# Optimization experiments

Measured on AMD Instinct MI355X. Metric: run time of the kernel, lower is better.

The kernel has to match this reference:

```python
import jax, jax.numpy as jnp
import numpy as np

DECAY = 0.99
EPS = 1e-05
LOSS_FACTOR = 0.1


def setup_inputs() -> dict:
    key = jax.random.key(0)
    k1, k2, k3, k4 = jax.random.split(key, 4)
    x = jax.random.normal(k1, (64, 256, 32, 32), dtype=jnp.float32)
    centroids = jax.random.normal(k2, (256, 1024), dtype=jnp.float32)
    cluster_size = jax.random.uniform(k3, (1024,), dtype=jnp.float32)
    centroids_avg = jax.random.normal(k4, (256, 1024), dtype=jnp.float32)
    return {"x": x, "centroids": centroids, "cluster_size": cluster_size,
            "centroids_avg": centroids_avg}


def _forward(x, centroids, cluster_size, centroids_avg):
    F, K = centroids.shape
    # torch: x_flat = x.transpose(-1, 1).contiguous().view(-1, n_features)
    xs = jnp.swapaxes(x, 1, -1)              # [B, W, H, C]
    flat_shape = xs.shape
    xf = xs.reshape(-1, F)                   # [N, F]
    dist = ((xf * xf).sum(1, keepdims=True)
            + (centroids * centroids).sum(0, keepdims=True)
            - 2.0 * (xf @ centroids))        # [N, K]
    ind = jnp.argmin(dist, axis=1)           # [N] nearest centroid
    # training-path EMA updates (one-hot matmuls expressed as segment sums)
    counts = jax.ops.segment_sum(jnp.ones(ind.shape, dtype=xf.dtype), ind,
                                 num_segments=K)              # [K]
    centroids_sum = jax.ops.segment_sum(xf, ind, num_segments=K).T  # [F, K]
    new_cs = DECAY * cluster_size + (1.0 - DECAY) * counts
    new_avg = DECAY * centroids_avg + (1.0 - DECAY) * centroids_sum
    n = new_cs.sum()
    cs_norm = (new_cs + EPS) / (n + K * EPS) * n
    new_centroids = new_avg / cs_norm[None, :]               # [F, K]
    # quantize with updated codebook (embedding lookup)
    xq = new_centroids.T[ind].reshape(flat_shape)            # [B, W, H, C]
    xq = jnp.swapaxes(xq, 1, -1)                             # [B, C, H, W]
    xq_st = x + jax.lax.stop_gradient(xq - x)                # straight-through
    return xq_st, xq


def reference(x, centroids, cluster_size, centroids_avg):
    out, _ = _forward(x, centroids, cluster_size, centroids_avg)
    return out
```

## Files before the change

kernel.cpp:

```cpp
#include <hip/hip_runtime.h>


#define DECAY 0.99f
#define EPSF 1e-5f
#define DELTA 0.05f

typedef _Float16 f16x8 __attribute__((ext_vector_type(8)));
typedef float f32x4 __attribute__((ext_vector_type(4)));

static __device__ __forceinline__ unsigned short h_bits(_Float16 h) {
  return __builtin_bit_cast(unsigned short, h);
}
static __device__ __forceinline__ float h_val(unsigned short u) {
  return (float)__builtin_bit_cast(_Float16, u);
}

__global__ void csq_kernel(const float* __restrict__ cent, float* __restrict__ csq) {
  int k0 = blockIdx.x * 64;
  int t = threadIdx.x;
  int kk = t & 63, cg = t >> 6;
  float s = 0.f;
  for (int c = cg; c < 256; c += 4) {
    float v = cent[(size_t)c * 1024 + k0 + kk];
    s += v * v;
  }
  __shared__ float red[4][64];
  red[cg][kk] = s;
  __syncthreads();
  if (t < 64) csq[k0 + t] = red[0][t] + red[1][t] + red[2][t] + red[3][t];
}

__global__ void centT_kernel(const float* __restrict__ cent, _Float16* __restrict__ ctp) {
  __shared__ float tl[32][33];
  int f0 = (blockIdx.x >> 5) * 32, k0 = (blockIdx.x & 31) * 32;
  int t = threadIdx.x;
#pragma unroll
  for (int i = 0; i < 4; ++i) {
    int fi = (t >> 5) + i * 8, ki = t & 31;
    tl[fi][ki] = cent[(size_t)(f0 + fi) * 1024 + k0 + ki];
  }
  __syncthreads();
#pragma unroll
  for (int i = 0; i < 4; ++i) {
    int ki = (t >> 5) + i * 8, fi = t & 31;
    int k = k0 + ki, f = f0 + fi;
    _Float16 h = (_Float16)tl[fi][ki];
    size_t idx = (size_t)(k >> 4) * 4096 + (size_t)(f >> 5) * 512 +
                 (size_t)(k & 15) * 32 + (size_t)((f >> 3) & 3) * 8 + (f & 7);
    ctp[idx] = h;
  }
}

__global__ void transpose_kernel(const float* __restrict__ x, _Float16* __restrict__ xh,
                                 _Float16* __restrict__ xl) {
  __shared__ float tile[64][65];
  int bid = blockIdx.x;
  int pt = bid & 15, ct = (bid >> 4) & 3, b = bid >> 6;
  int c0 = ct * 64, p0 = pt * 64;
  int t = threadIdx.x;
#pragma unroll
  for (int i = 0; i < 16; ++i) {
    int idx = t + i * 256;
    int ci = idx >> 6, pi = idx & 63;
    tile[ci][pi] = x[((size_t)(b * 256 + c0 + ci) << 10) + p0 + pi];
  }
  __syncthreads();
#pragma unroll
  for (int i = 0; i < 8; ++i) {
    int idx = t + i * 256;
    int pi = idx >> 5, cp = idx & 31;
    int p = p0 + pi;
    int r = ((p & 31) << 5) | (p >> 5);
    float v0 = tile[cp * 2][pi], v1 = tile[cp * 2 + 1][pi];
    _Float16 h0 = (_Float16)v0, h1 = (_Float16)v1;
    _Float16 l0 = (_Float16)(v0 - (float)h0), l1 = (_Float16)(v1 - (float)h1);
    unsigned int uh = (unsigned int)h_bits(h0) | ((unsigned int)h_bits(h1) << 16);
    unsigned int ul = (unsigned int)h_bits(l0) | ((unsigned int)h_bits(l1) << 16);
    size_t base = ((size_t)((b << 10) + r)) * 128 + ct * 32 + cp;
    ((unsigned int*)xh)[base] = uh;
    ((unsigned int*)xl)[base] = ul;
  }
}

__global__ __launch_bounds__(256, 2) void mfma_argmin_kernel(
    const _Float16* __restrict__ xh, const _Float16* __restrict__ ctp,
    const float* __restrict__ csq, int* __restrict__ ind,
    int* __restrict__ flaglist, unsigned int* __restrict__ flagcnt,
    unsigned int* __restrict__ counts) {
  __shared__ _Float16 Ah[64 * 256];
  __shared__ _Float16 Bst[4 * 2 * 4 * 512];
  __shared__ float csql[1024];
  __shared__ float red1[4][64], red2[4][64];
  __shared__ int redk[4][64];
  const int t = threadIdx.x;
  const int lane = t & 63, w = t >> 6;
  const int lr = lane & 15, lg = lane >> 4;
  const int n0 = blockIdx.x * 64;

#pragma unroll
  for (int i = 0; i < 4; ++i) csql[t + i * 256] = csq[t + i * 256];
#pragma unroll
  for (int i = 0; i < 8; ++i) {
    int idx = t + i * 256;
    int row = idx >> 5, c16 = (idx & 31) * 16;
    int sw = c16 ^ ((row & 7) << 4);
    *(f16x8*)((char*)Ah + row * 512 + sw) =
        *(const f16x8*)((const char*)xh + (size_t)(n0 + row) * 512 + c16);
  }
  __syncthreads();

  float b1[4][4], b2v[4][4];
  int bk[4][4];
#pragma unroll
  for (int rt = 0; rt < 4; ++rt)
#pragma unroll
    for (int rg = 0; rg < 4; ++rg) { b1[rt][rg] = 3.4e38f; b2v[rt][rg] = 3.4e38f; bk[rt][rg] = 0; }

  const int swz = (lr & 7) << 4;
  const int boffh = (lr * 4 + lg) * 8;
  const size_t lgo = (size_t)lane * 16;
  _Float16* bw = &Bst[w * 4096];

#define DMA4(CHB, KS, P)                                                              \
  do {                                                                                \
    const char* g_ = (const char*)ctp + (CHB) + (size_t)(KS) * 1024 + lgo;            \
    _Float16* l_ = bw + (P) * 2048;                                                   \
    __builtin_amdgcn_global_load_lds(                                                 \
        (const __attribute__((address_space(1))) unsigned int*)(g_),                  \
        (__attribute__((address_space(3))) unsigned int*)(l_), 16, 0, 0);             \
    __builtin_amdgcn_global_load_lds(                                                 \
        (const __attribute__((address_space(1))) unsigned int*)(g_ + 8192),           \
        (__attribute__((address_space(3))) unsigned int*)(l_ + 512), 16, 0, 0);       \
    __builtin_amdgcn_global_load_lds(                                                 \
        (const __attribute__((address_space(1))) unsigned int*)(g_ + 16384),          \
        (__attribute__((address_space(3))) unsigned int*)(l_ + 1024), 16, 0, 0);      \
    __builtin_amdgcn_global_load_lds(                                                 \
        (const __attribute__((address_space(1))) unsigned int*)(g_ + 24576),          \
        (__attribute__((address_space(3))) unsigned int*)(l_ + 1536), 16, 0, 0);      \
  } while (0)

#define KSHALF(KS, P, WN)                                                             \
  do {                                                                                \
    asm volatile("s_waitcnt vmcnt(" WN ")" ::: "memory");                             \
    __builtin_amdgcn_sched_barrier(0);                                                \
    const _Float16* bp_ = bw + (P) * 2048 + boffh;                                    \
    f16x8 q0 = *(const f16x8*)(bp_);                                                  \
    f16x8 q1 = *(const f16x8*)(bp_ + 512);                                            \
    f16x8 q2 = *(const f16x8*)(bp_ + 1024);                                           \
    f16x8 q3 = *(const f16x8*)(bp_ + 1536);                                           \
    const char* ap_ = (const char*)Ah + lr * 512 + (((KS) * 64 + lg * 16) ^ swz);     \
    f16x8 p0 = *(const f16x8*)(ap_);                                                  \
    f16x8 p1 = *(const f16x8*)(ap_ + 8192);                                           \
    f16x8 p2 = *(const f16x8*)(ap_ + 16384);                                          \
    f16x8 p3 = *(const f16x8*)(ap_ + 24576);                                          \
    acc[0][0] = __builtin_amdgcn_mfma_f32_16x16x32_f16(p0, q0, acc[0][0], 0, 0, 0);   \
    acc[0][1] = __builtin_amdgcn_mfma_f32_16x16x32_f16(p1, q0, acc[0][1], 0, 0, 0);   \
    acc[0][2] = __builtin_amdgcn_mfma_f32_16x16x32_f16(p2, q0, acc[0][2], 0, 0, 0);   \
    acc[0][3] = __builtin_amdgcn_mfma_f32_16x16x32_f16(p3, q0, acc[0][3], 0, 0, 0);   \
    acc[1][0] = __builtin_amdgcn_mfma_f32_16x16x32_f16(p0, q1, acc[1][0], 0, 0, 0);   \
    acc[1][1] = __builtin_amdgcn_mfma_f32_16x16x32_f16(p1, q1, acc[1][1], 0, 0, 0);   \
    acc[1][2] = __builtin_amdgcn_mfma_f32_16x16x32_f16(p2, q1, acc[1][2], 0, 0, 0);   \
    acc[1][3] = __builtin_amdgcn_mfma_f32_16x16x32_f16(p3, q1, acc[1][3], 0, 0, 0);   \
    acc[2][0] = __builtin_amdgcn_mfma_f32_16x16x32_f16(p0, q2, acc[2][0], 0, 0, 0);   \
    acc[2][1] = __builtin_amdgcn_mfma_f32_16x16x32_f16(p1, q2, acc[2][1], 0, 0, 0);   \
    acc[2][2] = __builtin_amdgcn_mfma_f32_16x16x32_f16(p2, q2, acc[2][2], 0, 0, 0);   \
    acc[2][3] = __builtin_amdgcn_mfma_f32_16x16x32_f16(p3, q2, acc[2][3], 0, 0, 0);   \
    acc[3][0] = __builtin_amdgcn_mfma_f32_16x16x32_f16(p0, q3, acc[3][0], 0, 0, 0);   \
    acc[3][1] = __builtin_amdgcn_mfma_f32_16x16x32_f16(p1, q3, acc[3][1], 0, 0, 0);   \
    acc[3][2] = __builtin_amdgcn_mfma_f32_16x16x32_f16(p2, q3, acc[3][2], 0, 0, 0);   \
    acc[3][3] = __builtin_amdgcn_mfma_f32_16x16x32_f16(p3, q3, acc[3][3], 0, 0, 0);   \
  } while (0)

  size_t chb = (size_t)w * 131072;
  DMA4(chb, 0, 0);
  DMA4(chb, 1, 1);
#pragma unroll 1
  for (int ch = 0; ch < 4; ++ch) {
    const int ccb = w * 256 + ch * 64;
    f32x4 acc[4][4];
#pragma unroll
    for (int ct = 0; ct < 4; ++ct)
#pragma unroll
      for (int rt = 0; rt < 4; ++rt) acc[ct][rt] = (f32x4){0.f, 0.f, 0.f, 0.f};

    KSHALF(0, 0, "4");  DMA4(chb, 2, 0);
    KSHALF(1, 1, "4");  DMA4(chb, 3, 1);
    KSHALF(2, 0, "4");  DMA4(chb, 4, 0);
    KSHALF(3, 1, "4");  DMA4(chb, 5, 1);
    KSHALF(4, 0, "4");  DMA4(chb, 6, 0);
    KSHALF(5, 1, "4");  DMA4(chb, 7, 1);
    KSHALF(6, 0, "4");
    if (ch < 3) {
      DMA4(chb + 32768, 0, 0);
      KSHALF(7, 1, "4");
      DMA4(chb + 32768, 1, 1);
    } else {
      KSHALF(7, 1, "0");
    }

#pragma unroll
    for (int ct = 0; ct < 4; ++ct) {
      const int col = ccb + ct * 16 + lr;
      const float cq = csql[col];
#pragma unroll
      for (int rt = 0; rt < 4; ++rt)
#pragma unroll
        for (int rg = 0; rg < 4; ++rg) {
          float d = cq - 2.f * acc[ct][rt][rg];
          if (d < b1[rt][rg]) {
            b2v[rt][rg] = b1[rt][rg];
            b1[rt][rg] = d;
            bk[rt][rg] = col;
          } else if (d < b2v[rt][rg]) {
            b2v[rt][rg] = d;
          }
        }
    }
    chb += 32768;
  }
#undef DMA4
#undef KSHALF

#pragma unroll
  for (int rt = 0; rt < 4; ++rt)
#pragma unroll
    for (int rg = 0; rg < 4; ++rg) {
      float v1 = b1[rt][rg], v2 = b2v[rt][rg];
      int kk = bk[rt][rg];
#pragma unroll
      for (int off = 8; off >= 1; off >>= 1) {
        float o1 = __shfl_xor(v1, off);
        int ok = __shfl_xor(kk, off);
        float o2 = __shfl_xor(v2, off);
        float nb2 = fminf(fmaxf(v1, o1), fminf(v2, o2));
        if (o1 < v1 || (o1 == v1 && ok < kk)) { v1 = o1; kk = ok; }
        v2 = nb2;
      }
      if (lr == 0) {
        int row = rt * 16 + lg * 4 + rg;
        red1[w][row] = v1;
        redk[w][row] = kk;
        red2[w][row] = v2;
      }
    }
  __syncthreads();
  if (t < 64) {
    float v1 = red1[0][t], v2 = red2[0][t];
    int kk = redk[0][t];
#pragma unroll
    for (int wi = 1; wi < 4; ++wi) {
      float o1 = red1[wi][t], o2 = red2[wi][t];
      int ok = redk[wi][t];
      float nb2 = fminf(fmaxf(v1, o1), fminf(v2, o2));
      if (o1 < v1 || (o1 == v1 && ok < kk)) { v1 = o1; kk = ok; }
      v2 = nb2;
    }
    ind[n0 + t] = kk;
    atomicAdd(&counts[kk], 1u);
    if (v2 - v1 < DELTA) {
      unsigned int p = atomicAdd(flagcnt, 1u);
      flaglist[p] = n0 + t;
    }
  }
}

__global__ __launch_bounds__(256) void fixup_kernel(
    const _Float16* __restrict__ xh, const _Float16* __restrict__ xl,
    const float* __restrict__ cent, const float* __restrict__ csq,
    const int* __restrict__ flaglist, const unsigned int* __restrict__ flagcnt,
    int* __restrict__ ind, unsigned int* __restrict__ counts) {
  const int t = threadIdx.x;
  const int nf = (int)*flagcnt;
  __shared__ float xrow[256];
  __shared__ float rv[256];
  __shared__ int rk[256];
  for (int ii = blockIdx.x; ii < nf; ii += gridDim.x) {
    __syncthreads();
    int row = flaglist[ii];
    xrow[t] = (float)xh[(size_t)row * 256 + t] + (float)xl[(size_t)row * 256 + t];
    __syncthreads();
    float a0 = 0.f, a1 = 0.f, a2 = 0.f, a3 = 0.f;
#pragma unroll 8
    for (int f = 0; f < 256; ++f) {
      float xs = xrow[f];
      const float* cr = cent + (size_t)f * 1024 + t;
      a0 += xs * cr[0];
      a1 += xs * cr[256];
      a2 += xs * cr[512];
      a3 += xs * cr[768];
    }
    float bd = csq[t] - 2.f * a0;
    int bkk = t;
    float d1 = csq[t + 256] - 2.f * a1;
    if (d1 < bd) { bd = d1; bkk = t + 256; }
    float d2 = csq[t + 512] - 2.f * a2;
    if (d2 < bd) { bd = d2; bkk = t + 512; }
    float d3 = csq[t + 768] - 2.f * a3;
    if (d3 < bd) { bd = d3; bkk = t + 768; }
    rv[t] = bd;
    rk[t] = bkk;
    __syncthreads();
    for (int off = 128; off >= 1; off >>= 1) {
      if (t < off) {
        float ov = rv[t + off];
        int ok = rk[t + off];
        if (ov < rv[t] || (ov == rv[t] && ok < rk[t])) { rv[t] = ov; rk[t] = ok; }
      }
      __syncthreads();
    }
    if (t == 0) {
      int newk = rk[0];
      int oldk = ind[row];
      if (newk != oldk) {
        ind[row] = newk;
        atomicAdd(&counts[oldk], 0xFFFFFFFFu);
        atomicAdd(&counts[newk], 1u);
      }
    }
  }
}

__global__ __launch_bounds__(64) void csnorm_scan_kernel(
    const float* __restrict__ cs, const unsigned int* __restrict__ counts,
    float* __restrict__ icn, unsigned int* __restrict__ offsets,
    unsigned int* __restrict__ cursor) {
  const int t = threadIdx.x;
  unsigned int cl[16];
  float csl[16];
  unsigned int s = 0;
  float css = 0.f;
#pragma unroll
  for (int j = 0; j < 16; ++j) {
    cl[j] = counts[t * 16 + j];
    s += cl[j];
    csl[j] = cs[t * 16 + j];
    css += csl[j];
  }
  unsigned int incl = s;
#pragma unroll
  for (int off = 1; off < 64; off <<= 1) {
    unsigned int v = __shfl_up(incl, off);
    if (t >= off) incl += v;
  }
  unsigned int run = incl - s;
  float tot = css;
#pragma unroll
  for (int off = 32; off >= 1; off >>= 1) tot += __shfl_xor(tot, off);
  const float n = DECAY * tot + (1.f - DECAY) * 65536.f;
#pragma unroll
  for (int j = 0; j < 16; ++j) {
    int k = t * 16 + j;
    offsets[k] = run;
    cursor[k] = run;
    float ncs = DECAY * csl[j] + (1.f - DECAY) * (float)cl[j];
    float csn = (ncs + EPSF) / (n + 1024.f * EPSF) * n;
    icn[k] = 1.f / csn;
    run += cl[j];
  }
  if (t == 63) offsets[1024] = run;
}

__global__ void scatter_kernel(const int* __restrict__ ind, unsigned int* __restrict__ cursor,
                               int* __restrict__ rowlist) {
  int n = blockIdx.x * 256 + threadIdx.x;
  int k = ind[n];
  unsigned int pos = atomicAdd(&cursor[k], 1u);
  rowlist[pos] = n;
}

__global__ __launch_bounds__(256) void sumflush_kernel(
    const _Float16* __restrict__ xh, const int* __restrict__ rowlist,
    const int* __restrict__ ind, float* __restrict__ sums) {
  __shared__ int rl[64];
  __shared__ int kl[64];
  const int t = threadIdx.x;
  const int sub = t >> 6, lane = t & 63;
  const int p0 = blockIdx.x * 64;
  if (t < 64) {
    int r = rowlist[p0 + t];
    rl[t] = r;
    kl[t] = ind[r];
  }
  __syncthreads();
  float a0 = 0.f, a1 = 0.f, a2 = 0.f, a3 = 0.f;
  int curk = kl[sub * 16];
#pragma unroll
  for (int i = 0; i < 16; ++i) {
    int p = sub * 16 + i;
    int k = kl[p];
    if (k != curk) {
      float* dst = &sums[(size_t)curk * 256 + lane * 4];
      atomicAdd(&dst[0], a0);
      atomicAdd(&dst[1], a1);
      atomicAdd(&dst[2], a2);
      atomicAdd(&dst[3], a3);
      a0 = a1 = a2 = a3 = 0.f;
      curk = k;
    }
    int r = rl[p];
    uint2 vh = *(const uint2*)&((const unsigned int*)xh)[(size_t)r * 128 + lane * 2];
    a0 += h_val((unsigned short)(vh.x & 0xFFFF));
    a1 += h_val((unsigned short)(vh.x >> 16));
    a2 += h_val((unsigned short)(vh.y & 0xFFFF));
    a3 += h_val((unsigned short)(vh.y >> 16));
  }
  float* dst = &sums[(size_t)curk * 256 + lane * 4];
  atomicAdd(&dst[0], a0);
  atomicAdd(&dst[1], a1);
  atomicAdd(&dst[2], a2);
  atomicAdd(&dst[3], a3);
}

__global__ __launch_bounds__(256) void newcentT_kernel(
    const float* __restrict__ sums, const float* __restrict__ avg,
    const float* __restrict__ icn, float* __restrict__ nc) {
  __shared__ float tl[32][33];
  const int t = threadIdx.x;
  const int k0 = (blockIdx.x & 31) * 32, f0 = (blockIdx.x >> 5) * 32;
#pragma unroll
  for (int i = 0; i < 4; ++i) {
    int ki = (t >> 5) + i * 8, fi = t & 31;
    tl[ki][fi] = sums[(size_t)(k0 + ki) * 256 + f0 + fi];
  }
  __syncthreads();
#pragma unroll
  for (int i = 0; i < 4; ++i) {
    int fi = (t >> 5) + i * 8, ki = t & 31;
    size_t idx = (size_t)(f0 + fi) * 1024 + k0 + ki;
    nc[idx] = (DECAY * avg[idx] + (1.f - DECAY) * tl[ki][fi]) * icn[k0 + ki];
  }
}

__global__ void gather_kernel(const float* __restrict__ nc, const int* __restrict__ ind,
                              float* __restrict__ out) {
  __shared__ int ip[1024];
  int b = blockIdx.x >> 3;
  int cg = (blockIdx.x & 7) * 32;
  int t = threadIdx.x;
#pragma unroll
  for (int j = 0; j < 4; ++j) {
    int p = t + j * 256;
    int r = ((p & 31) << 5) | (p >> 5);
    ip[p] = ind[(b << 10) + r];
  }
  __syncthreads();
  for (int c = cg; c < cg + 32; ++c) {
    const float* row = nc + (size_t)c * 1024;
#pragma unroll
    for (int j = 0; j < 4; ++j) {
      int p = t + j * 256;
      out[((size_t)(b * 256 + c) << 10) + p] = row[ip[p]];
    }
  }
}

extern "C" void kernel_launch(void* const* d_in, const int* in_sizes, int n_in,
                              void* d_out, int out_size, void* d_ws, size_t ws_size,
                              hipStream_t stream) {
  const float* x = (const float*)d_in[0];
  const float* cent = (const float*)d_in[1];
  const float* cs = (const float*)d_in[2];
  const float* avg = (const float*)d_in[3];
  float* out = (float*)d_out;

  char* ws = (char*)d_ws;
  _Float16* xh = (_Float16*)ws;
  _Float16* xl = (_Float16*)(ws + 33554432);
  _Float16* ctp = (_Float16*)(ws + 67108864);
  float* nc = (float*)(ws + 67108864);
  unsigned int* counts = (unsigned int*)(ws + 68157440);
  unsigned int* flagcnt = (unsigned int*)(ws + 68161536);
  float* sums = (float*)(ws + 68165632);
  float* csqv = (float*)(ws + 69214208);
  float* icn = (float*)(ws + 69218304);
  unsigned int* offsets = (unsigned int*)(ws + 69222400);
  unsigned int* cursor = (unsigned int*)(ws + 69230592);
  int* ind = (int*)(ws + 69234688);
  int* flaglist = (int*)(ws + 69496832);
  int* rowlist = (int*)(ws + 69496832);

  hipMemsetAsync(counts, 0, 1056768, stream);

  csq_kernel<<<16, 256, 0, stream>>>(cent, csqv);
  centT_kernel<<<256, 256, 0, stream>>>(cent, ctp);
  transpose_kernel<<<4096, 256, 0, stream>>>(x, xh, xl);
  mfma_argmin_kernel<<<1024, 256, 0, stream>>>(xh, ctp, csqv, ind, flaglist, flagcnt, counts);
  fixup_kernel<<<128, 256, 0, stream>>>(xh, xl, cent, csqv, flaglist, flagcnt, ind, counts);
  csnorm_scan_kernel<<<1, 64, 0, stream>>>(cs, counts, icn, offsets, cursor);
  scatter_kernel<<<256, 256, 0, stream>>>(ind, cursor, rowlist);
  sumflush_kernel<<<1024, 256, 0, stream>>>(xh, rowlist, ind, sums);
  newcentT_kernel<<<256, 256, 0, stream>>>(sums, avg, icn, nc);
  gather_kernel<<<512, 256, 0, stream>>>(nc, ind, out);
}
```

Measured before the change: 277.9 us.

## Drop fp16 low-part buffer, fuse csq and zeroing, batch fixup rows, vectorize gather

The transpose now writes only the fp16 high part, and the fixup kernel reads exact fp32 rows straight from x. That removes a 32 MB workspace write. The csq computation and the counter zeroing move into the centroid-transpose kernel, and the sums buffer is zeroed inside scatter, which removes the memset and one launch. Fixup processes four flagged rows per block with 256 blocks so each centroid load is reused, and gather writes float4 stores. The trade-off is strided reads of x in fixup and more registers per fixup thread.

```diff
diff --git a/kernel.cpp b/kernel.cpp
--- a/kernel.cpp
+++ b/kernel.cpp
@@ -15,25 +15,13 @@
   return (float)__builtin_bit_cast(_Float16, u);
 }
 
-__global__ void csq_kernel(const float* __restrict__ cent, float* __restrict__ csq) {
-  int k0 = blockIdx.x * 64;
-  int t = threadIdx.x;
-  int kk = t & 63, cg = t >> 6;
-  float s = 0.f;
-  for (int c = cg; c < 256; c += 4) {
-    float v = cent[(size_t)c * 1024 + k0 + kk];
-    s += v * v;
-  }
-  __shared__ float red[4][64];
-  red[cg][kk] = s;
-  __syncthreads();
-  if (t < 64) csq[k0 + t] = red[0][t] + red[1][t] + red[2][t] + red[3][t];
-}
-
-__global__ void centT_kernel(const float* __restrict__ cent, _Float16* __restrict__ ctp) {
+__global__ void centT_kernel(const float* __restrict__ cent, _Float16* __restrict__ ctp,
+                             float* __restrict__ csq, unsigned int* __restrict__ counts,
+                             unsigned int* __restrict__ flagcnt) {
   __shared__ float tl[32][33];
-  int f0 = (blockIdx.x >> 5) * 32, k0 = (blockIdx.x & 31) * 32;
-  int t = threadIdx.x;
+  const int bid = blockIdx.x;
+  const int f0 = (bid >> 5) * 32, k0 = (bid & 31) * 32;
+  const int t = threadIdx.x;
 #pragma unroll
   for (int i = 0; i < 4; ++i) {
     int fi = (t >> 5) + i * 8, ki = t & 31;
@@ -49,10 +37,34 @@
                  (size_t)(k & 15) * 32 + (size_t)((f >> 3) & 3) * 8 + (f & 7);
     ctp[idx] = h;
   }
-}
-
-__global__ void transpose_kernel(const float* __restrict__ x, _Float16* __restrict__ xh,
-                                 _Float16* __restrict__ xl) {
+  if (bid < 32) {
+    __shared__ float red[8][32];
+    const int kk = k0 + (t & 31);
+    const int fg = t >> 5;
+    float s = 0.f;
+    for (int f = fg * 32; f < fg * 32 + 32; ++f) {
+      float v = cent[(size_t)f * 1024 + kk];
+      s += v * v;
+    }
+    red[fg][t & 31] = s;
+    __syncthreads();
+    if (t < 32) {
+      float tot = 0.f;
+#pragma unroll
+      for (int g = 0; g < 8; ++g) tot += red[g][t];
+      csq[k0 + t] = tot;
+    }
+  }
+  if (bid == 32) {
+    counts[t] = 0u;
+    counts[t + 256] = 0u;
+    counts[t + 512] = 0u;
+    counts[t + 768] = 0u;
+    if (t == 0) *flagcnt = 0u;
+  }
+}
+
+__global__ void transpose_kernel(const float* __restrict__ x, _Float16* __restrict__ xh) {
   __shared__ float tile[64][65];
   int bid = blockIdx.x;
   int pt = bid & 15, ct = (bid >> 4) & 3, b = bid >> 6;
@@ -72,13 +84,9 @@
     int p = p0 + pi;
     int r = ((p & 31) << 5) | (p >> 5);
     float v0 = tile[cp * 2][pi], v1 = tile[cp * 2 + 1][pi];
-    _Float16 h0 = (_Float16)v0, h1 = (_Float16)v1;
-    _Float16 l0 = (_Float16)(v0 - (float)h0), l1 = (_Float16)(v1 - (float)h1);
-    unsigned int uh = (unsigned int)h_bits(h0) | ((unsigned int)h_bits(h1) << 16);
-    unsigned int ul = (unsigned int)h_bits(l0) | ((unsigned int)h_bits(l1) << 16);
-    size_t base = ((size_t)((b << 10) + r)) * 128 + ct * 32 + cp;
-    ((unsigned int*)xh)[base] = uh;
-    ((unsigned int*)xl)[base] = ul;
+    unsigned int uh = (unsigned int)h_bits((_Float16)v0) |
+                      ((unsigned int)h_bits((_Float16)v1) << 16);
+    ((unsigned int*)xh)[((size_t)((b << 10) + r)) * 128 + ct * 32 + cp] = uh;
   }
 }
 
@@ -265,57 +273,75 @@
 }
 
 __global__ __launch_bounds__(256) void fixup_kernel(
-    const _Float16* __restrict__ xh, const _Float16* __restrict__ xl,
-    const float* __restrict__ cent, const float* __restrict__ csq,
-    const int* __restrict__ flaglist, const unsigned int* __restrict__ flagcnt,
-    int* __restrict__ ind, unsigned int* __restrict__ counts) {
+    const float* __restrict__ x, const float* __restrict__ cent,
+    const float* __restrict__ csq, const int* __restrict__ flaglist,
+    const unsigned int* __restrict__ flagcnt, int* __restrict__ ind,
+    unsigned int* __restrict__ counts) {
   const int t = threadIdx.x;
   const int nf = (int)*flagcnt;
-  __shared__ float xrow[256];
+  __shared__ float xrow[4][256];
+  __shared__ int rows[4];
   __shared__ float rv[256];
   __shared__ int rk[256];
-  for (int ii = blockIdx.x; ii < nf; ii += gridDim.x) {
+  for (int base = blockIdx.x * 4; base < nf; base += gridDim.x * 4) {
+    const int cnt = min(4, nf - base);
     __syncthreads();
-    int row = flaglist[ii];
-    xrow[t] = (float)xh[(size_t)row * 256 + t] + (float)xl[(size_t)row * 256 + t];
+    if (t < 4) rows[t] = flaglist[base + (t < cnt ? t : 0)];
     __syncthreads();
-    float a0 = 0.f, a1 = 0.f, a2 = 0.f, a3 = 0.f;
-#pragma unroll 8
+#pragma unroll
+    for (int j = 0; j < 4; ++j) {
+      int row = rows[j];
+      int b = row >> 10, r = row & 1023, wq = r >> 5, h = r & 31;
+      xrow[j][t] = x[((size_t)(b * 256 + t) << 10) + h * 32 + wq];
+    }
+    __syncthreads();
+    float a[4][4];
+#pragma unroll
+    for (int j = 0; j < 4; ++j)
+#pragma unroll
+      for (int q = 0; q < 4; ++q) a[j][q] = 0.f;
+#pragma unroll 4
     for (int f = 0; f < 256; ++f) {
-      float xs = xrow[f];
       const float* cr = cent + (size_t)f * 1024 + t;
-      a0 += xs * cr[0];
-      a1 += xs * cr[256];
-      a2 += xs * cr[512];
-      a3 += xs * cr[768];
-    }
-    float bd = csq[t] - 2.f * a0;
-    int bkk = t;
-    float d1 = csq[t + 256] - 2.f * a1;
-    if (d1 < bd) { bd = d1; bkk = t + 256; }
-    float d2 = csq[t + 512] - 2.f * a2;
-    if (d2 < bd) { bd = d2; bkk = t + 512; }
-    float d3 = csq[t + 768] - 2.f * a3;
-    if (d3 < bd) { bd = d3; bkk = t + 768; }
-    rv[t] = bd;
-    rk[t] = bkk;
-    __syncthreads();
-    for (int off = 128; off >= 1; off >>= 1) {
-      if (t < off) {
-        float ov = rv[t + off];
-        int ok = rk[t + off];
-        if (ov < rv[t] || (ov == rv[t] && ok < rk[t])) { rv[t] = ov; rk[t] = ok; }
+      float c0 = cr[0], c1 = cr[256], c2 = cr[512], c3 = cr[768];
+#pragma unroll
+      for (int j = 0; j < 4; ++j) {
+        float xv = xrow[j][f];
+        a[j][0] += xv * c0;
+        a[j][1] += xv * c1;
+        a[j][2] += xv * c2;
+        a[j][3] += xv * c3;
+      }
+    }
+    for (int j = 0; j < cnt; ++j) {
+      float bd = csq[t] - 2.f * a[j][0];
+      int bkk = t;
+      float d1 = csq[t + 256] - 2.f * a[j][1];
+      if (d1 < bd) { bd = d1; bkk = t + 256; }
+      float d2 = csq[t + 512] - 2.f * a[j][2];
+      if (d2 < bd) { bd = d2; bkk = t + 512; }
+      float d3 = csq[t + 768] - 2.f * a[j][3];
+      if (d3 < bd) { bd = d3; bkk = t + 768; }
+      rv[t] = bd;
+      rk[t] = bkk;
+      __syncthreads();
+      for (int off = 128; off >= 1; off >>= 1) {
+        if (t < off) {
+          float ov = rv[t + off];
+          int ok = rk[t + off];
+          if (ov < rv[t] || (ov == rv[t] && ok < rk[t])) { rv[t] = ov; rk[t] = ok; }
+        }
+        __syncthreads();
+      }
+      if (t == 0) {
+        int newk = rk[0], row = rows[j], oldk = ind[row];
+        if (newk != oldk) {
+          ind[row] = newk;
+          atomicAdd(&counts[oldk], 0xFFFFFFFFu);
+          atomicAdd(&counts[newk], 1u);
+        }
       }
       __syncthreads();
-    }
-    if (t == 0) {
-      int newk = rk[0];
-      int oldk = ind[row];
-      if (newk != oldk) {
-        ind[row] = newk;
-        atomicAdd(&counts[oldk], 0xFFFFFFFFu);
-        atomicAdd(&counts[newk], 1u);
-      }
     }
   }
 }
@@ -361,8 +387,9 @@
 }
 
 __global__ void scatter_kernel(const int* __restrict__ ind, unsigned int* __restrict__ cursor,
-                               int* __restrict__ rowlist) {
+                               int* __restrict__ rowlist, float4* __restrict__ sums4) {
   int n = blockIdx.x * 256 + threadIdx.x;
+  sums4[n] = (float4){0.f, 0.f, 0.f, 0.f};
   int k = ind[n];
   unsigned int pos = atomicAdd(&cursor[k], 1u);
   rowlist[pos] = n;
@@ -444,13 +471,12 @@
     ip[p] = ind[(b << 10) + r];
   }
   __syncthreads();
+  const int p0 = t * 4;
+  const int i0 = ip[p0], i1 = ip[p0 + 1], i2 = ip[p0 + 2], i3 = ip[p0 + 3];
   for (int c = cg; c < cg + 32; ++c) {
     const float* row = nc + (size_t)c * 1024;
-#pragma unroll
-    for (int j = 0; j < 4; ++j) {
-      int p = t + j * 256;
-      out[((size_t)(b * 256 + c) << 10) + p] = row[ip[p]];
-    }
+    float4 v = {row[i0], row[i1], row[i2], row[i3]};
+    *(float4*)&out[((size_t)(b * 256 + c) << 10) + p0] = v;
   }
 }
 
@@ -465,29 +491,25 @@
 
   char* ws = (char*)d_ws;
   _Float16* xh = (_Float16*)ws;
-  _Float16* xl = (_Float16*)(ws + 33554432);
-  _Float16* ctp = (_Float16*)(ws + 67108864);
-  float* nc = (float*)(ws + 67108864);
-  unsigned int* counts = (unsigned int*)(ws + 68157440);
-  unsigned int* flagcnt = (unsigned int*)(ws + 68161536);
-  float* sums = (float*)(ws + 68165632);
-  float* csqv = (float*)(ws + 69214208);
-  float* icn = (float*)(ws + 69218304);
-  unsigned int* offsets = (unsigned int*)(ws + 69222400);
-  unsigned int* cursor = (unsigned int*)(ws + 69230592);
-  int* ind = (int*)(ws + 69234688);
-  int* flaglist = (int*)(ws + 69496832);
-  int* rowlist = (int*)(ws + 69496832);
-
-  hipMemsetAsync(counts, 0, 1056768, stream);
-
-  csq_kernel<<<16, 256, 0, stream>>>(cent, csqv);
-  centT_kernel<<<256, 256, 0, stream>>>(cent, ctp);
-  transpose_kernel<<<4096, 256, 0, stream>>>(x, xh, xl);
+  _Float16* ctp = (_Float16*)(ws + 33554432);
+  float* nc = (float*)(ws + 33554432);
+  unsigned int* counts = (unsigned int*)(ws + 34603008);
+  unsigned int* flagcnt = (unsigned int*)(ws + 34607104);
+  float* csqv = (float*)(ws + 34611200);
+  float* icn = (float*)(ws + 34615296);
+  unsigned int* offsets = (unsigned int*)(ws + 34619392);
+  unsigned int* cursor = (unsigned int*)(ws + 34627584);
+  int* ind = (int*)(ws + 34631680);
+  int* flaglist = (int*)(ws + 34893824);
+  int* rowlist = (int*)(ws + 34893824);
+  float* sums = (float*)(ws + 35155968);
+
+  centT_kernel<<<256, 256, 0, stream>>>(cent, ctp, csqv, counts, flagcnt);
+  transpose_kernel<<<4096, 256, 0, stream>>>(x, xh);
   mfma_argmin_kernel<<<1024, 256, 0, stream>>>(xh, ctp, csqv, ind, flaglist, flagcnt, counts);
-  fixup_kernel<<<128, 256, 0, stream>>>(xh, xl, cent, csqv, flaglist, flagcnt, ind, counts);
+  fixup_kernel<<<256, 256, 0, stream>>>(x, cent, csqv, flaglist, flagcnt, ind, counts);
   csnorm_scan_kernel<<<1, 64, 0, stream>>>(cs, counts, icn, offsets, cursor);
-  scatter_kernel<<<256, 256, 0, stream>>>(ind, cursor, rowlist);
+  scatter_kernel<<<256, 256, 0, stream>>>(ind, cursor, rowlist, (float4*)sums);
   sumflush_kernel<<<1024, 256, 0, stream>>>(xh, rowlist, ind, sums);
   newcentT_kernel<<<256, 256, 0, stream>>>(sums, avg, icn, nc);
   gather_kernel<<<512, 256, 0, stream>>>(nc, ind, out);
```

Result: faster. 265.2 us (-4.5%).
